# Kernel tuning notes

Measured on AMD Instinct MI355X. Metric: run time of the kernel, lower is better.

The kernel has to match this reference:

```python
import jax, jax.numpy as jnp
import numpy as np

DIM_HEAD = 64
NB_FEATURES = 256
COND_LEN = 128
NUM_CHUNKS = 128  # torch .chunk(128, dim=-2) -> 128 chunks
KERNEL_EPS = 1e-4
ATTN_EPS = 1e-6


def gaussian_orthogonal_random_matrix(key, nb_rows, nb_cols):
    # scaling == 0 branch of the torch code
    nb_full = nb_rows // nb_cols
    blocks = []
    for i in range(nb_full + (1 if nb_rows % nb_cols else 0)):
        g = jax.random.normal(jax.random.fold_in(key, i), (nb_cols, nb_cols), dtype=jnp.float32)
        qm, _ = jnp.linalg.qr(g)
        blocks.append(qm.T)
    final = jnp.concatenate(blocks, axis=0)[:nb_rows]
    mult = jnp.linalg.norm(
        jax.random.normal(jax.random.fold_in(key, 10_000), (nb_rows, nb_cols), dtype=jnp.float32), axis=1)
    return mult[:, None] * final  # diag(mult) @ final


def softmax_kernel(x, proj, is_query):
    d = x.shape[-1]
    data_normalizer = d ** (-0.25)
    ratio = proj.shape[0] ** (-0.5)
    # [b,h,n,m]
    data_dash = jnp.einsum('bhnd,md->bhnm', data_normalizer * x, proj)
    diag = (x * x).sum(-1) * 0.5 * (data_normalizer ** 2)  # [b,h,n]
    diag = diag[..., None]
    if is_query:
        m = jnp.max(data_dash, axis=-1, keepdims=True)
    else:
        m = jnp.max(data_dash)
    return ratio * (jnp.exp(data_dash - diag - m) + KERNEL_EPS)


def causal_linear_attention(qf, kf, v):
    b, h, s, m = qf.shape
    e = v.shape[-1]
    # conditioning prefix: non-causal linear attention
    cq, ck, cv = qf[:, :, :COND_LEN], kf[:, :, :COND_LEN], v[:, :, :COND_LEN]
    cond_k_sum = ck.sum(axis=-2)                                   # [b,h,m]
    cond_Dinv = 1.0 / jnp.einsum('bhnd,bhd->bhn', cq, cond_k_sum)
    cond_ctx = jnp.einsum('bhnd,bhne->bhde', ck, cv)               # [b,h,m,e]
    cond_out = jnp.einsum('bhde,bhnd,bhn->bhne', cond_ctx, cq, cond_Dinv)

    # causal chunked recurrence over the remainder
    rest = s - COND_LEN
    L = rest // NUM_CHUNKS
    def to_chunks(t):
        return t[:, :, COND_LEN:].reshape(b, h, NUM_CHUNKS, L, t.shape[-1]).transpose(2, 0, 1, 3, 4)
    qr, kr, vr = to_chunks(qf), to_chunks(kf), to_chunks(v)

    def step(carry, qkv):
        last_k, last_ctx = carry  # [b,h,m], [b,h,m,e]
        qc, kc, vc = qkv          # [b,h,L,m], [b,h,L,m], [b,h,L,e]
        k_cumsum = last_k[:, :, None, :] + jnp.cumsum(kc, axis=-2)
        D_inv = 1.0 / jnp.einsum('bhld,bhld->bhl', qc, k_cumsum + ATTN_EPS)
        ctx = jnp.einsum('bhld,bhle->bhlde', kc, vc)
        ctx_cumsum = last_ctx[:, :, None] + jnp.cumsum(ctx, axis=-3)
        out = jnp.einsum('bhlde,bhld,bhl->bhle', ctx_cumsum, qc, D_inv)
        return (k_cumsum[:, :, -1], ctx_cumsum[:, :, -1]), out

    _, outs = jax.lax.scan(step, (cond_k_sum, cond_ctx), (qr, kr, vr))
    outs = outs.transpose(1, 2, 0, 3, 4).reshape(b, h, rest, e)
    return jnp.concatenate([cond_out, outs], axis=2)


def setup_inputs() -> dict:
    key = jax.random.key(0)
    kq, kk, kv, kp = jax.random.split(key, 4)
    B, H, S = 4, 16, 4096
    q = jax.random.normal(kq, (B, H, S, DIM_HEAD), dtype=jnp.float32)
    k = jax.random.normal(kk, (B, H, S, DIM_HEAD), dtype=jnp.float32)
    v = jax.random.normal(kv, (B, H, S, DIM_HEAD), dtype=jnp.float32)
    projection_matrix = gaussian_orthogonal_random_matrix(kp, NB_FEATURES, DIM_HEAD)
    return {"q": q, "k": k, "v": v, "projection_matrix": projection_matrix}


def reference(q, k, v, projection_matrix):
    qf = softmax_kernel(q, projection_matrix, is_query=True)
    kf = softmax_kernel(k, projection_matrix, is_query=False)
    return causal_linear_attention(qf, kf, v)
```

## Files before the change

### kernel.cpp

```cpp
#include <hip/hip_runtime.h>
#include <math.h>


#define S_TOT 4096
#define CONDL 128
#define SLOT_F 16640
#define RATIO 0.0625f
#define DNORM 0.35355339059327378f
#define KEPS  1e-4f
#define AEPS  1e-6f

typedef __attribute__((ext_vector_type(8))) short bf16x8;
typedef __attribute__((ext_vector_type(2))) unsigned uint2v;
typedef __attribute__((ext_vector_type(4))) float f32x4;

#define MFMA16(a,b,c) __builtin_amdgcn_mfma_f32_16x16x32_bf16(a,b,c,0,0,0)

static __device__ __forceinline__ unsigned cvtpk(float a, float b){
    unsigned r;
    asm("v_cvt_pk_bf16_f32 %0, %1, %2" : "=v"(r) : "v"(a), "v"(b));
    return r;
}
static __device__ __forceinline__ float lo16f(unsigned u){ return __uint_as_float(u << 16); }
static __device__ __forceinline__ float hi16f(unsigned u){ return __uint_as_float(u & 0xffff0000u); }

static __device__ __forceinline__ unsigned short f2bh(float x){
    unsigned u = __float_as_uint(x);
    u += 0x7fffu + ((u >> 16) & 1u);
    return (unsigned short)(u >> 16);
}
static __device__ __forceinline__ float bh2f(unsigned short h){
    return __uint_as_float((unsigned)h << 16);
}
static __device__ __forceinline__ unsigned packhl(float x){
    unsigned u1 = cvtpk(x, x);
    float r = x - lo16f(u1);
    return cvtpk(x, r);
}
static __device__ __forceinline__ void unpk(const uint4 a, const uint4 b, bf16x8& h, bf16x8& l){
    h[0]=(short)a.x; h[1]=(short)a.y; h[2]=(short)a.z; h[3]=(short)a.w;
    h[4]=(short)b.x; h[5]=(short)b.y; h[6]=(short)b.z; h[7]=(short)b.w;
    l[0]=(short)(a.x>>16); l[1]=(short)(a.y>>16); l[2]=(short)(a.z>>16); l[3]=(short)(a.w>>16);
    l[4]=(short)(b.x>>16); l[5]=(short)(b.y>>16); l[6]=(short)(b.z>>16); l[7]=(short)(b.w>>16);
}
static __device__ __forceinline__ unsigned mapf(float x){
    unsigned u = __float_as_uint(x);
    return (u & 0x80000000u) ? ~u : (u | 0x80000000u);
}
static __device__ __forceinline__ float unmapf(unsigned u){
    return __uint_as_float((u & 0x80000000u) ? (u ^ 0x80000000u) : ~u);
}

static __device__ __forceinline__ void conv_write(const float* __restrict__ Xg, long r0,
        int tid, short (*Xh)[64][8], short (*Xl)[64][8], float* __restrict__ diag_)
{
    int row = tid >> 4;
    int c4  = (tid & 15) * 4;
    float4 x4 = *(const float4*)(Xg + (r0 + row)*64 + c4);
    float x0 = x4.x*DNORM, x1 = x4.y*DNORM, x2 = x4.z*DNORM, x3 = x4.w*DNORM;
    float ss = x0*x0 + x1*x1 + x2*x2 + x3*x3;
    ss += __shfl_xor(ss, 1, 64);
    ss += __shfl_xor(ss, 2, 64);
    ss += __shfl_xor(ss, 4, 64);
    ss += __shfl_xor(ss, 8, 64);
    if ((tid & 15) == 0) diag_[row] = 0.5f * ss;
    int rt = row >> 4, lr = row & 15;
    int kk = c4 >> 5, c5 = c4 & 31;
    int fg, j0;
    if (c5 < 16){ fg = c5 >> 2; j0 = 0; } else { fg = (c5 - 16) >> 2; j0 = 4; }
    int f = kk*2 + rt;
    unsigned a01 = cvtpk(x0, x1), a23 = cvtpk(x2, x3);
    unsigned b01 = cvtpk(x0 - lo16f(a01), x1 - hi16f(a01));
    unsigned b23 = cvtpk(x2 - lo16f(a23), x3 - hi16f(a23));
    uint2v hv, lv;
    hv[0] = a01; hv[1] = a23;
    lv[0] = b01; lv[1] = b23;
    *(uint2v*)&Xh[f][fg*16 + lr][j0] = hv;
    *(uint2v*)&Xl[f][fg*16 + lr][j0] = lv;
}

static __device__ __forceinline__ void load_pfrags(const unsigned short* __restrict__ Ph,
        const unsigned short* __restrict__ Pl, int w, int l15, int g,
        bf16x8 (&Pfh)[2][2], bf16x8 (&Pfl)[2][2])
{
#pragma unroll
    for (int mt=0; mt<2; mt++)
#pragma unroll
      for (int kk=0; kk<2; kk++){
        const unsigned short* ph = Ph + (w*32 + mt*16 + l15)*64 + kk*32 + g*4;
        const unsigned short* pl = Pl + (w*32 + mt*16 + l15)*64 + kk*32 + g*4;
        bf16x8 fh, fl;
#pragma unroll
        for (int j=0;j<4;j++){
            fh[j]=(short)ph[j]; fh[4+j]=(short)ph[16+j];
            fl[j]=(short)pl[j]; fl[4+j]=(short)pl[16+j];
        }
        Pfh[mt][kk]=fh; Pfl[mt][kk]=fl;
      }
}

static __device__ __forceinline__ void dd_frags(const short (*Xh)[64][8], const short (*Xl)[64][8],
        int lane, const bf16x8 (&Pfh)[2][2], const bf16x8 (&Pfl)[2][2], f32x4 (&acc)[2][2])
{
#pragma unroll
    for (int rt=0;rt<2;rt++)
#pragma unroll
      for (int mt=0;mt<2;mt++) acc[rt][mt] = f32x4{0.f,0.f,0.f,0.f};
#pragma unroll
    for (int kk=0;kk<2;kk++)
#pragma unroll
      for (int rt=0;rt<2;rt++){
        bf16x8 xh = *(const bf16x8*)&Xh[kk*2+rt][lane][0];
        bf16x8 xl = *(const bf16x8*)&Xl[kk*2+rt][lane][0];
#pragma unroll
        for (int mt=0;mt<2;mt++){
            acc[rt][mt] = MFMA16(xh, Pfh[mt][kk], acc[rt][mt]);
            acc[rt][mt] = MFMA16(xh, Pfl[mt][kk], acc[rt][mt]);
            acc[rt][mt] = MFMA16(xl, Pfh[mt][kk], acc[rt][mt]);
        }
      }
}

static __device__ __forceinline__ void dd_frags_g(const short (*Xh)[64][8], const short (*Xl)[64][8],
        int lane, int w, const unsigned short* __restrict__ Pfh, const unsigned short* __restrict__ Pfl,
        f32x4 (&acc)[2][2])
{
#pragma unroll
    for (int rr=0;rr<2;rr++)
#pragma unroll
      for (int mt=0;mt<2;mt++) acc[rr][mt] = f32x4{0.f,0.f,0.f,0.f};
#pragma unroll
    for (int kk=0;kk<2;kk++){
        bf16x8 ph[2], pl[2];
#pragma unroll
        for (int mt=0;mt<2;mt++){
            int f = w*4 + kk*2 + mt;
            ph[mt] = *(const bf16x8*)(Pfh + (f*64 + lane)*8);
            pl[mt] = *(const bf16x8*)(Pfl + (f*64 + lane)*8);
        }
#pragma unroll
        for (int rr=0;rr<2;rr++){
            bf16x8 xh = *(const bf16x8*)&Xh[kk*2+rr][lane][0];
            bf16x8 xl = *(const bf16x8*)&Xl[kk*2+rr][lane][0];
#pragma unroll
            for (int mt=0;mt<2;mt++){
                acc[rr][mt] = MFMA16(xh, ph[mt], acc[rr][mt]);
                acc[rr][mt] = MFMA16(xh, pl[mt], acc[rr][mt]);
                acc[rr][mt] = MFMA16(xl, ph[mt], acc[rr][mt]);
            }
        }
    }
}

static __device__ __forceinline__ void sfrag(const f32x4 a, const f32x4 b, bf16x8& h, bf16x8& l){
    union U { bf16x8 v; unsigned u[4]; } H, L;
    H.u[0] = cvtpk(a[0], a[1]); H.u[1] = cvtpk(a[2], a[3]);
    H.u[2] = cvtpk(b[0], b[1]); H.u[3] = cvtpk(b[2], b[3]);
    L.u[0] = cvtpk(a[0] - lo16f(H.u[0]), a[1] - hi16f(H.u[0]));
    L.u[1] = cvtpk(a[2] - lo16f(H.u[1]), a[3] - hi16f(H.u[1]));
    L.u[2] = cvtpk(b[0] - lo16f(H.u[2]), b[1] - hi16f(H.u[2]));
    L.u[3] = cvtpk(b[2] - lo16f(H.u[3]), b[3] - hi16f(H.u[3]));
    h = H.v; l = L.v;
}

static __device__ __forceinline__ void inter_half(const unsigned* __restrict__ qf_,
        const f32x4 (&S)[8], int rt, int l15, int g, int xsw,
        f32x4 &Cp0, f32x4 &Cp1)
{
#pragma unroll
    for (int ktl=0; ktl<4; ktl++){
        int ft = rt*4 + ktl;
        bf16x8 sh, sl; sfrag(S[2*ktl], S[2*ktl+1], sh, sl);
        {
            int rowb = l15*256;
            uint4 q0 = *(const uint4*)&qf_[rowb + ((ft*32 + g*4) ^ xsw)];
            uint4 q1 = *(const uint4*)&qf_[rowb + ((ft*32 + 16 + g*4) ^ xsw)];
            bf16x8 qh, ql; unpk(q0, q1, qh, ql);
            Cp0 = MFMA16(qh, sh, Cp0);
            Cp0 = MFMA16(qh, sl, Cp0);
            Cp0 = MFMA16(ql, sh, Cp0);
        }
        {
            int rowb = (16 + l15)*256;
            uint4 q0 = *(const uint4*)&qf_[rowb + ((ft*32 + g*4) ^ xsw)];
            uint4 q1 = *(const uint4*)&qf_[rowb + ((ft*32 + 16 + g*4) ^ xsw)];
            bf16x8 qh, ql; unpk(q0, q1, qh, ql);
            Cp1 = MFMA16(qh, sh, Cp1);
            Cp1 = MFMA16(qh, sl, Cp1);
            Cp1 = MFMA16(ql, sh, Cp1);
        }
    }
}

__global__ __launch_bounds__(256) void init_p_kernel(const float* __restrict__ proj,
        unsigned short* __restrict__ Ph, unsigned short* __restrict__ Pl,
        unsigned short* __restrict__ Pfh, unsigned short* __restrict__ Pfl){
    int i = blockIdx.x*256 + threadIdx.x;
    float x = proj[i];
    unsigned short h = f2bh(x);
    unsigned short l = f2bh(x - bh2f(h));
    Ph[i] = h;
    Pl[i] = l;
    int m = i >> 6, d = i & 63;
    int w = m >> 5, mt = (m >> 4) & 1, l15 = m & 15;
    int kk = d >> 5, r5 = d & 31;
    int half = r5 >> 4, g = (r5 & 15) >> 2, jj = r5 & 3;
    int f = w*4 + kk*2 + mt, lane = g*16 + l15, j = half*4 + jj;
    int o = (f*64 + lane)*8 + j;
    Pfh[o] = h; Pfl[o] = l;
}

__global__ __launch_bounds__(256) void kmax_kernel(const float* __restrict__ k,
        const unsigned short* __restrict__ Ph, unsigned* __restrict__ kmax_u){
    __shared__ float red[4];
    int tid = threadIdx.x;
    int lane = tid & 63, w = tid >> 6;
    int l15 = lane & 15, g = lane >> 4;
    long r0 = (long)blockIdx.x * 32;
    bf16x8 xh[2][2];
#pragma unroll
    for (int kk=0;kk<2;kk++)
#pragma unroll
      for (int rt=0;rt<2;rt++){
        const float* rp = k + (r0 + rt*16 + l15)*64 + kk*32 + g*4;
        float4 a = *(const float4*)rp;
        float4 b = *(const float4*)(rp + 16);
        float xs[8] = {a.x,a.y,a.z,a.w,b.x,b.y,b.z,b.w};
#pragma unroll
        for (int j=0;j<8;j++) xh[kk][rt][j] = (short)f2bh(xs[j]*DNORM);
      }
    float mx = -1e30f;
#pragma unroll
    for (int mtl=0; mtl<4; mtl++){
        int mtile = w*4 + mtl;
        bf16x8 pf[2];
#pragma unroll
        for (int kk=0;kk<2;kk++){
            const unsigned short* ph = Ph + (mtile*16 + l15)*64 + kk*32 + g*4;
#pragma unroll
            for (int j=0;j<4;j++){ pf[kk][j]=(short)ph[j]; pf[kk][4+j]=(short)ph[16+j]; }
        }
        f32x4 acc[2] = {f32x4{0.f,0.f,0.f,0.f}, f32x4{0.f,0.f,0.f,0.f}};
#pragma unroll
        for (int kk=0;kk<2;kk++)
#pragma unroll
          for (int rt=0;rt<2;rt++)
            acc[rt] = MFMA16(xh[kk][rt], pf[kk], acc[rt]);
#pragma unroll
        for (int rt=0;rt<2;rt++)
#pragma unroll
          for (int i=0;i<4;i++) mx = fmaxf(mx, acc[rt][i]);
    }
#pragma unroll
    for (int d=1; d<64; d<<=1) mx = fmaxf(mx, __shfl_xor(mx, d, 64));
    if (lane == 0) red[w] = mx;
    __syncthreads();
    if (tid == 0){
        float m2 = fmaxf(fmaxf(red[0],red[1]), fmaxf(red[2],red[3]));
        atomicMax(kmax_u, mapf(m2));
    }
}

__global__ __launch_bounds__(512, 2) void b_kernel(const float* __restrict__ k,
        const float* __restrict__ v,
        const unsigned short* __restrict__ Ph, const unsigned short* __restrict__ Pl,
        const unsigned* __restrict__ kmax_u, float* __restrict__ states,
        int CH, int nch){
    __shared__ short Xh[4][64][8], Xl[4][64][8];
    __shared__ unsigned kf_mt[256][36];
    __shared__ unsigned Vt_u[64][36];
    __shared__ float diagk_[32];
    int tid = threadIdx.x;
    int lane = tid & 63, w = tid >> 6;
    int l15 = lane & 15, g = lane >> 4;
    int cx = blockIdx.x, bh = blockIdx.y;
    int o = (cx == 0) ? 0 : CONDL + (cx-1)*CH;
    int nsub = ((cx == 0) ? CONDL : CH) >> 5;
    long rowbase = (long)bh * S_TOT + o;
    float kmax = unmapf(*kmax_u);
    bf16x8 Pfh[2][2], Pfl[2][2];
    load_pfrags(Ph, Pl, w, l15, g, Pfh, Pfl);
    f32x4 Sacc[2][4];
#pragma unroll
    for (int mt=0;mt<2;mt++)
#pragma unroll
      for (int et=0;et<4;et++) Sacc[mt][et] = f32x4{0.f,0.f,0.f,0.f};
    float zacc[2] = {0.f, 0.f};

    for (int st = 0; st < nsub; st++){
        long r0 = rowbase + st*32;
        conv_write(k, r0, tid, Xh, Xl, diagk_);
        {
            int t = tid >> 4, e4 = (tid & 15)*4;
            float4 v4 = *(const float4*)(v + (r0 + t)*64 + e4);
            Vt_u[e4+0][t] = packhl(v4.x);
            Vt_u[e4+1][t] = packhl(v4.y);
            Vt_u[e4+2][t] = packhl(v4.z);
            Vt_u[e4+3][t] = packhl(v4.w);
        }
        __syncthreads();
        f32x4 dk[2][2];
        dd_frags(Xh, Xl, lane, Pfh, Pfl, dk);
        float zd[2] = {0.f, 0.f};
#pragma unroll
        for (int rt=0;rt<2;rt++)
#pragma unroll
          for (int i=0;i<4;i++){
            int t = rt*16 + g*4 + i;
            float dg = diagk_[t];
#pragma unroll
            for (int mt=0;mt<2;mt++){
                float kv = RATIO * (__expf(dk[rt][mt][i] - dg - kmax) + KEPS);
                kf_mt[w*32 + mt*16 + l15][t] = packhl(kv);
                zd[mt] += kv;
            }
          }
#pragma unroll
        for (int mt=0;mt<2;mt++){
            zd[mt] += __shfl_xor(zd[mt], 16, 64);
            zd[mt] += __shfl_xor(zd[mt], 32, 64);
            zacc[mt] += zd[mt];
        }
        __syncthreads();
#pragma unroll
        for (int mt=0;mt<2;mt++){
            int m = (w*2 + mt)*16 + l15;
            const uint4* kp0 = (const uint4*)&kf_mt[m][g*4];
            const uint4* kp1 = (const uint4*)&kf_mt[m][16 + g*4];
            bf16x8 kh, kl; unpk(*kp0, *kp1, kh, kl);
#pragma unroll
            for (int et=0;et<4;et++){
                const uint4* vp0 = (const uint4*)&Vt_u[et*16 + l15][g*4];
                const uint4* vp1 = (const uint4*)&Vt_u[et*16 + l15][16 + g*4];
                bf16x8 vh, vl; unpk(*vp0, *vp1, vh, vl);
                Sacc[mt][et] = MFMA16(kh, vh, Sacc[mt][et]);
                Sacc[mt][et] = MFMA16(kh, vl, Sacc[mt][et]);
                Sacc[mt][et] = MFMA16(kl, vh, Sacc[mt][et]);
            }
        }
        __syncthreads();
    }
    float* Sg = states + ((long)(bh*nch + cx)) * SLOT_F;
#pragma unroll
    for (int mt=0;mt<2;mt++)
#pragma unroll
      for (int et=0;et<4;et++)
#pragma unroll
        for (int i=0;i<4;i++)
            Sg[((w*2+mt)*16 + g*4 + i)*64 + et*16 + l15] = Sacc[mt][et][i];
    if (g == 0){
        Sg[16384 + w*32 + l15]      = zacc[0];
        Sg[16384 + w*32 + 16 + l15] = zacc[1];
    }
}

__global__ __launch_bounds__(256) void scan_kernel(float* __restrict__ states, int nch){
    int idx = blockIdx.x*256 + threadIdx.x;
    if (idx >= SLOT_F) return;
    float* base = states + (long)blockIdx.y * nch * SLOT_F + idx;
    float prev = 0.f;
    for (int c = 0; c < nch; c++){
        float t = base[(long)c * SLOT_F];
        base[(long)c * SLOT_F] = prev;
        prev += t;
    }
}

__global__ __launch_bounds__(512, 2) void d_kernel(const float* __restrict__ q,
        const float* __restrict__ k, const float* __restrict__ v,
        const unsigned short* __restrict__ Pfh, const unsigned short* __restrict__ Pfl,
        const unsigned* __restrict__ kmax_u, const float* __restrict__ states,
        float* __restrict__ out, int CH, int nch){
    __shared__ __attribute__((aligned(16))) unsigned lds_[18496];
    unsigned* qf_ = lds_;
    unsigned* kf_ = lds_ + 8192;
    unsigned* XA_ = lds_ + 16384;
    float*   den_ = (float*)(lds_ + 18432);
    float*   dgk_ = (float*)(lds_ + 18464);
    float*   dgq_ = (float*)kf_;
    unsigned* rmax_ = kf_ + 32;
    unsigned* A_ = XA_;
    float*   xch_ = (float*)(lds_ + 17408);
    short (*Xh)[64][8] = (short (*)[64][8])XA_;
    short (*Xl)[64][8] = (short (*)[64][8])(XA_ + 1024);

    int tid = threadIdx.x;
    int lane = tid & 63, w = tid >> 6;
    int l15 = lane & 15, g = lane >> 4;
    int et = w & 3, rt = w >> 2;
    bool owner = (rt == 0);
    int cx = blockIdx.x, bh = blockIdx.y;
    bool causal = (cx > 0);
    int o = causal ? (CONDL + (cx-1)*CH) : 0;
    int nsub = (causal ? CH : CONDL) >> 5;
    float epsv = causal ? AEPS : 0.f;
    int slot = causal ? cx : 1;
    const float* Sg = states + ((long)(bh*nch + slot)) * SLOT_F;
    long rowbase = (long)bh * S_TOT + o;
    float kmax = unmapf(*kmax_u);
    int xsw = (l15 & 7) << 2;

    f32x4 S[8];
#pragma unroll
    for (int Mtl=0; Mtl<8; Mtl++){
#pragma unroll
        for (int i=0;i<4;i++)
            S[Mtl][i] = Sg[((rt*8 + Mtl)*16 + g*4 + i)*64 + et*16 + l15];
    }
    float z0 = Sg[16384 + w*32 + l15];
    float z1 = Sg[16384 + w*32 + 16 + l15];

    for (int st = 0; st < nsub; st++){
        long r0 = rowbase + st*32;
        conv_write(q, r0, tid, Xh, Xl, dgq_);
        if (tid < 32){ den_[tid] = 0.f; rmax_[tid] = 0u; }
        __syncthreads();
        f32x4 dq[2][2];
        dd_frags_g(Xh, Xl, lane, w, Pfh, Pfl, dq);
#pragma unroll
        for (int rr=0;rr<2;rr++)
#pragma unroll
          for (int i=0;i<4;i++){
            float mx = fmaxf(dq[rr][0][i], dq[rr][1][i]);
            mx = fmaxf(mx, __shfl_xor(mx, 1, 64));
            mx = fmaxf(mx, __shfl_xor(mx, 2, 64));
            mx = fmaxf(mx, __shfl_xor(mx, 4, 64));
            mx = fmaxf(mx, __shfl_xor(mx, 8, 64));
            if (l15 == 0) atomicMax(&rmax_[rr*16 + g*4 + i], mapf(mx));
          }
        __syncthreads();
        {
#pragma unroll
            for (int rr=0;rr<2;rr++)
#pragma unroll
              for (int i=0;i<4;i++){
                int row = rr*16 + g*4 + i;
                float dgv = dgq_[row];
                float rm = unmapf(rmax_[row]);
                float s1p = 0.f, s2p = 0.f;
#pragma unroll
                for (int mt=0;mt<2;mt++){
                    float qv = RATIO * (__expf(dq[rr][mt][i] - dgv - rm) + KEPS);
                    s1p += qv;
                    s2p += qv * (mt ? z1 : z0);
                    int m = w*32 + mt*16 + l15;
                    qf_[row*256 + (m ^ ((row & 7) << 2))] = packhl(qv);
                }
#pragma unroll
                for (int d2=1; d2<16; d2<<=1){
                    s1p += __shfl_xor(s1p, d2, 64);
                    s2p += __shfl_xor(s2p, d2, 64);
                }
                if (l15 == 0) atomicAdd(&den_[row], s2p + epsv * s1p);
              }
        }
        if (causal) conv_write(k, r0, tid, Xh, Xl, dgk_);
        __syncthreads();
        if (causal){
            f32x4 dk[2][2];
            dd_frags_g(Xh, Xl, lane, w, Pfh, Pfl, dk);
            float zd0 = 0.f, zd1 = 0.f;
#pragma unroll
            for (int rr=0;rr<2;rr++){
                float dg0 = dgk_[rr*16 + g*4 + 0];
                float dg1 = dgk_[rr*16 + g*4 + 1];
                float dg2 = dgk_[rr*16 + g*4 + 2];
                float dg3 = dgk_[rr*16 + g*4 + 3];
#pragma unroll
                for (int mt=0;mt<2;mt++){
                    float k0 = RATIO * (__expf(dk[rr][mt][0] - dg0 - kmax) + KEPS);
                    float k1 = RATIO * (__expf(dk[rr][mt][1] - dg1 - kmax) + KEPS);
                    float k2 = RATIO * (__expf(dk[rr][mt][2] - dg2 - kmax) + KEPS);
                    float k3 = RATIO * (__expf(dk[rr][mt][3] - dg3 - kmax) + KEPS);
                    if (mt == 0) zd0 += k0+k1+k2+k3; else zd1 += k0+k1+k2+k3;
                    uint4 kw;
                    kw.x = packhl(k0); kw.y = packhl(k1);
                    kw.z = packhl(k2); kw.w = packhl(k3);
                    int m = w*32 + mt*16 + l15;
                    *(uint4*)&kf_[m*32 + ((rr*16 + g*4) ^ xsw)] = kw;
                }
            }
            zd0 += __shfl_xor(zd0, 16, 64); zd0 += __shfl_xor(zd0, 32, 64);
            zd1 += __shfl_xor(zd1, 16, 64); zd1 += __shfl_xor(zd1, 32, 64);
            z0 += zd0; z1 += zd1;
        }
        __syncthreads();
        float vv[8];
        if (causal){
            const float* vb = v + r0*64 + et*16 + l15;
#pragma unroll
            for (int p2=0;p2<2;p2++)
#pragma unroll
              for (int j=0;j<4;j++)
                vv[p2*4+j] = vb[(p2*16 + g*4 + j)*64];
        }
        f32x4 Cp0{0.f,0.f,0.f,0.f}, Cp1{0.f,0.f,0.f,0.f};
        if (owner){
            if (causal){
                int ar = et >> 1, tt = et & 1;
                f32x4 c{0.f,0.f,0.f,0.f};
                int rowb = (ar*16 + l15)*256;
#pragma unroll
                for (int kt=0;kt<8;kt++){
                    uint4 q0 = *(const uint4*)&qf_[rowb + ((kt*32 + g*4) ^ xsw)];
                    uint4 q1 = *(const uint4*)&qf_[rowb + ((kt*32 + 16 + g*4) ^ xsw)];
                    bf16x8 qh, ql; unpk(q0, q1, qh, ql);
                    bf16x8 kh, kl;
#pragma unroll
                    for (int p2=0;p2<2;p2++)
#pragma unroll
                      for (int j=0;j<4;j++){
                        int m = kt*32 + p2*16 + g*4 + j;
                        unsigned u = kf_[m*32 + ((tt*16 + l15) ^ ((m & 7) << 2))];
                        kh[p2*4+j] = (short)u;
                        kl[p2*4+j] = (short)(u >> 16);
                      }
                    c = MFMA16(qh, kh, c);
                    c = MFMA16(qh, kl, c);
                    c = MFMA16(ql, kh, c);
                }
                int t = tt*16 + l15;
#pragma unroll
                for (int i=0;i<4;i++){
                    int r = ar*16 + g*4 + i;
                    float a = (t <= r) ? c[i] : 0.f;
                    A_[r*32 + (t ^ ((r & 7) << 2))] = packhl(a);
                    float p = a;
                    p += __shfl_xor(p, 1, 64);
                    p += __shfl_xor(p, 2, 64);
                    p += __shfl_xor(p, 4, 64);
                    p += __shfl_xor(p, 8, 64);
                    if (l15 == 0) atomicAdd(&den_[r], p);
                }
            }
        } else {
            inter_half(qf_, S, rt, l15, g, xsw, Cp0, Cp1);
            *(float4*)&xch_[(et*64 + lane)*4] = float4{Cp0[0],Cp0[1],Cp0[2],Cp0[3]};
        }
        __syncthreads();
        if (owner){
            inter_half(qf_, S, rt, l15, g, xsw, Cp0, Cp1);
            float4 pp = *(const float4*)&xch_[(et*64 + lane)*4];
            Cp0[0] += pp.x; Cp0[1] += pp.y; Cp0[2] += pp.z; Cp0[3] += pp.w;
            *(float4*)&xch_[(et*64 + lane)*4] = float4{Cp1[0],Cp1[1],Cp1[2],Cp1[3]};
        }
        if (causal){
            f32x4 va{vv[0], vv[1], vv[2], vv[3]};
            f32x4 vb2{vv[4], vv[5], vv[6], vv[7]};
            bf16x8 vh, vl; sfrag(va, vb2, vh, vl);
#pragma unroll
            for (int Mtl=0;Mtl<8;Mtl++){
                int mb = ((rt*8 + Mtl)*16 + l15)*32;
                uint4 k0 = *(const uint4*)&kf_[mb + ((g*4) ^ xsw)];
                uint4 k1 = *(const uint4*)&kf_[mb + ((16 + g*4) ^ xsw)];
                bf16x8 kh, kl; unpk(k0, k1, kh, kl);
                S[Mtl] = MFMA16(kh, vh, S[Mtl]);
                S[Mtl] = MFMA16(kh, vl, S[Mtl]);
                S[Mtl] = MFMA16(kl, vh, S[Mtl]);
            }
            int rb = (rt*16 + l15)*32;
            uint4 a0 = *(const uint4*)&A_[rb + ((g*4) ^ xsw)];
            uint4 a1 = *(const uint4*)&A_[rb + ((16 + g*4) ^ xsw)];
            bf16x8 ah, al; unpk(a0, a1, ah, al);
            f32x4& Ct = owner ? Cp0 : Cp1;
            Ct = MFMA16(ah, vh, Ct);
            Ct = MFMA16(ah, vl, Ct);
            Ct = MFMA16(al, vh, Ct);
        }
        if (owner){
#pragma unroll
            for (int i=0;i<4;i++){
                int row = g*4 + i;
                out[(r0 + row)*64 + et*16 + l15] = Cp0[i] / den_[row];
            }
        }
        __syncthreads();
        if (!owner){
            float4 pp = *(const float4*)&xch_[(et*64 + lane)*4];
            Cp1[0] += pp.x; Cp1[1] += pp.y; Cp1[2] += pp.z; Cp1[3] += pp.w;
#pragma unroll
            for (int i=0;i<4;i++){
                int row = 16 + g*4 + i;
                out[(r0 + row)*64 + et*16 + l15] = Cp1[i] / den_[row];
            }
        }
        __syncthreads();
    }
}

extern "C" void kernel_launch(void* const* d_in, const int* in_sizes, int n_in,
                              void* d_out, int out_size, void* d_ws, size_t ws_size,
                              hipStream_t stream) {
    const float* q = (const float*)d_in[0];
    const float* k = (const float*)d_in[1];
    const float* v = (const float*)d_in[2];
    const float* proj = (const float*)d_in[3];
    float* out = (float*)d_out;

    unsigned* kmax_u = (unsigned*)d_ws;
    unsigned short* Ph  = (unsigned short*)((char*)d_ws + 256);
    unsigned short* Pl  = Ph + 16384;
    unsigned short* Pfh = Pl + 16384;
    unsigned short* Pfl = Pfh + 16384;
    float* states = (float*)((char*)d_ws + 256 + 131072);
    size_t fixed = 256 + 131072;

    int CH, nch;
    size_t need128 = fixed + (size_t)64 * 32 * SLOT_F * 4;
    if (ws_size >= need128){ CH = 128; nch = 32; }
    else                  { CH = 992; nch = 5;  }

    hipMemsetAsync(d_ws, 0, 4, stream);
    hipLaunchKernelGGL(init_p_kernel, dim3(64), dim3(256), 0, stream, proj, Ph, Pl, Pfh, Pfl);
    hipLaunchKernelGGL(kmax_kernel, dim3(8192), dim3(256), 0, stream, k, Ph, kmax_u);
    hipLaunchKernelGGL(b_kernel, dim3(nch, 64), dim3(512), 0, stream, k, v, Ph, Pl, kmax_u, states, CH, nch);
    hipLaunchKernelGGL(scan_kernel, dim3(65, 64), dim3(256), 0, stream, states, nch);
    hipLaunchKernelGGL(d_kernel, dim3(nch, 64), dim3(512), 0, stream, q, k, v, Pfh, Pfl, kmax_u, states, out, CH, nch);
}
```

Measured before the change: 639.6 us.

## Split bf16 hi/lo planes in LDS and add transposed K feature copy

Stores q/k features and the intra-chunk A matrix in LDS as separate high and low bf16 planes, with k-major index permutations. MFMA operands can then be loaded as contiguous 16-byte vectors instead of being unpacked from interleaved hi/lo words. A transposed copy of the k features is also written so the QK^T product reads contiguous rows rather than gathering 16 scalar LDS reads per fragment. The LDS footprint grows to about 107 KB and launch bounds drop to one block per CU, so occupancy falls in exchange for fewer LDS instructions and less unpack work.

```diff
diff --git a/kernel.cpp b/kernel.cpp
--- a/kernel.cpp
+++ b/kernel.cpp
@@ -163,28 +163,26 @@
     h = H.v; l = L.v;
 }
 
-static __device__ __forceinline__ void inter_half(const unsigned* __restrict__ qf_,
-        const f32x4 (&S)[8], int rt, int l15, int g, int xsw,
+static __device__ __forceinline__ void inter_half(const unsigned short* __restrict__ qfh_,
+        const unsigned short* __restrict__ qfl_,
+        const f32x4 (&S)[8], int rt, int l15, int g, int xq,
         f32x4 &Cp0, f32x4 &Cp1)
 {
 #pragma unroll
     for (int ktl=0; ktl<4; ktl++){
         int ft = rt*4 + ktl;
         bf16x8 sh, sl; sfrag(S[2*ktl], S[2*ktl+1], sh, sl);
+        int fo = (ft*32 + g*8) ^ xq;
         {
-            int rowb = l15*256;
-            uint4 q0 = *(const uint4*)&qf_[rowb + ((ft*32 + g*4) ^ xsw)];
-            uint4 q1 = *(const uint4*)&qf_[rowb + ((ft*32 + 16 + g*4) ^ xsw)];
-            bf16x8 qh, ql; unpk(q0, q1, qh, ql);
+            bf16x8 qh = *(const bf16x8*)&qfh_[l15*256 + fo];
+            bf16x8 ql = *(const bf16x8*)&qfl_[l15*256 + fo];
             Cp0 = MFMA16(qh, sh, Cp0);
             Cp0 = MFMA16(qh, sl, Cp0);
             Cp0 = MFMA16(ql, sh, Cp0);
         }
         {
-            int rowb = (16 + l15)*256;
-            uint4 q0 = *(const uint4*)&qf_[rowb + ((ft*32 + g*4) ^ xsw)];
-            uint4 q1 = *(const uint4*)&qf_[rowb + ((ft*32 + 16 + g*4) ^ xsw)];
-            bf16x8 qh, ql; unpk(q0, q1, qh, ql);
+            bf16x8 qh = *(const bf16x8*)&qfh_[(16 + l15)*256 + fo];
+            bf16x8 ql = *(const bf16x8*)&qfl_[(16 + l15)*256 + fo];
             Cp1 = MFMA16(qh, sh, Cp1);
             Cp1 = MFMA16(qh, sl, Cp1);
             Cp1 = MFMA16(ql, sh, Cp1);
@@ -366,23 +364,27 @@
     }
 }
 
-__global__ __launch_bounds__(512, 2) void d_kernel(const float* __restrict__ q,
+__global__ __launch_bounds__(512, 1) void d_kernel(const float* __restrict__ q,
         const float* __restrict__ k, const float* __restrict__ v,
         const unsigned short* __restrict__ Pfh, const unsigned short* __restrict__ Pfl,
         const unsigned* __restrict__ kmax_u, const float* __restrict__ states,
         float* __restrict__ out, int CH, int nch){
-    __shared__ __attribute__((aligned(16))) unsigned lds_[18496];
-    unsigned* qf_ = lds_;
-    unsigned* kf_ = lds_ + 8192;
-    unsigned* XA_ = lds_ + 16384;
-    float*   den_ = (float*)(lds_ + 18432);
-    float*   dgk_ = (float*)(lds_ + 18464);
-    float*   dgq_ = (float*)kf_;
-    unsigned* rmax_ = kf_ + 32;
-    unsigned* A_ = XA_;
-    float*   xch_ = (float*)(lds_ + 17408);
-    short (*Xh)[64][8] = (short (*)[64][8])XA_;
-    short (*Xl)[64][8] = (short (*)[64][8])(XA_ + 1024);
+    __shared__ __attribute__((aligned(16))) unsigned short hws[53504];
+    unsigned short* qfh_ = hws;
+    unsigned short* qfl_ = hws + 8192;
+    unsigned short* kfh_ = hws + 16384;
+    unsigned short* kfl_ = hws + 24576;
+    unsigned short* kfTh_ = hws + 32768;
+    unsigned short* kfTl_ = hws + 40960;
+    short (*Xh)[64][8] = (short (*)[64][8])(hws + 49152);
+    short (*Xl)[64][8] = (short (*)[64][8])(hws + 51200);
+    unsigned short* Ah_ = hws + 49152;
+    unsigned short* Al_ = hws + 50176;
+    float* xch_ = (float*)(hws + 51200);
+    float* den_ = (float*)(hws + 53248);
+    float* dgq_ = (float*)(hws + 53312);
+    float* dgk_ = (float*)(hws + 53376);
+    unsigned* rmax_ = (unsigned*)(hws + 53440);
 
     int tid = threadIdx.x;
     int lane = tid & 63, w = tid >> 6;
@@ -398,7 +400,9 @@
     const float* Sg = states + ((long)(bh*nch + slot)) * SLOT_F;
     long rowbase = (long)bh * S_TOT + o;
     float kmax = unmapf(*kmax_u);
-    int xsw = (l15 & 7) << 2;
+    int xq = (l15 & 7) << 3;
+    int xk = (l15 & 3) << 3;
+    int pbase = w*32 + ((l15 >> 2) << 3) + (l15 & 3);
 
     f32x4 S[8];
 #pragma unroll
@@ -437,14 +441,19 @@
                 int row = rr*16 + g*4 + i;
                 float dgv = dgq_[row];
                 float rm = unmapf(rmax_[row]);
+                int xrow = ((g*4 + i) & 7) << 3;
                 float s1p = 0.f, s2p = 0.f;
 #pragma unroll
                 for (int mt=0;mt<2;mt++){
                     float qv = RATIO * (__expf(dq[rr][mt][i] - dgv - rm) + KEPS);
                     s1p += qv;
                     s2p += qv * (mt ? z1 : z0);
-                    int m = w*32 + mt*16 + l15;
-                    qf_[row*256 + (m ^ ((row & 7) << 2))] = packhl(qv);
+                    unsigned hu = cvtpk(qv, qv);
+                    float lres = qv - lo16f(hu);
+                    unsigned lu = cvtpk(lres, lres);
+                    int idx = row*256 + ((pbase + mt*4) ^ xrow);
+                    qfh_[idx] = (unsigned short)hu;
+                    qfl_[idx] = (unsigned short)lu;
                 }
 #pragma unroll
                 for (int d2=1; d2<16; d2<<=1){
@@ -473,11 +482,26 @@
                     float k2 = RATIO * (__expf(dk[rr][mt][2] - dg2 - kmax) + KEPS);
                     float k3 = RATIO * (__expf(dk[rr][mt][3] - dg3 - kmax) + KEPS);
                     if (mt == 0) zd0 += k0+k1+k2+k3; else zd1 += k0+k1+k2+k3;
-                    uint4 kw;
-                    kw.x = packhl(k0); kw.y = packhl(k1);
-                    kw.z = packhl(k2); kw.w = packhl(k3);
+                    unsigned h01 = cvtpk(k0, k1), h23 = cvtpk(k2, k3);
+                    float l0 = k0 - lo16f(h01), l1 = k1 - hi16f(h01);
+                    float l2 = k2 - lo16f(h23), l3 = k3 - hi16f(h23);
+                    unsigned L01 = cvtpk(l0, l1), L23 = cvtpk(l2, l3);
                     int m = w*32 + mt*16 + l15;
-                    *(uint4*)&kf_[m*32 + ((rr*16 + g*4) ^ xsw)] = kw;
+                    int bidx = m*32 + ((g*8 + rr*4) ^ xk);
+                    uint2v hv; hv[0] = h01; hv[1] = h23;
+                    *(uint2v*)&kfh_[bidx] = hv;
+                    uint2v lv2; lv2[0] = L01; lv2[1] = L23;
+                    *(uint2v*)&kfl_[bidx] = lv2;
+                    int pm = pbase + mt*4;
+                    int t0 = rr*16 + g*4;
+                    kfTh_[(t0+0)*256 + (pm ^ ((((g*4)+0)&7)<<3))] = (unsigned short)h01;
+                    kfTh_[(t0+1)*256 + (pm ^ ((((g*4)+1)&7)<<3))] = (unsigned short)(h01>>16);
+                    kfTh_[(t0+2)*256 + (pm ^ ((((g*4)+2)&7)<<3))] = (unsigned short)h23;
+                    kfTh_[(t0+3)*256 + (pm ^ ((((g*4)+3)&7)<<3))] = (unsigned short)(h23>>16);
+                    kfTl_[(t0+0)*256 + (pm ^ ((((g*4)+0)&7)<<3))] = (unsigned short)L01;
+                    kfTl_[(t0+1)*256 + (pm ^ ((((g*4)+1)&7)<<3))] = (unsigned short)(L01>>16);
+                    kfTl_[(t0+2)*256 + (pm ^ ((((g*4)+2)&7)<<3))] = (unsigned short)L23;
+                    kfTl_[(t0+3)*256 + (pm ^ ((((g*4)+3)&7)<<3))] = (unsigned short)(L23>>16);
                 }
             }
             zd0 += __shfl_xor(zd0, 16, 64); zd0 += __shfl_xor(zd0, 32, 64);
@@ -498,33 +522,31 @@
         if (owner){
             if (causal){
                 int ar = et >> 1, tt = et & 1;
+                int t = tt*16 + l15;
+                int rowA = ar*16 + l15;
                 f32x4 c{0.f,0.f,0.f,0.f};
-                int rowb = (ar*16 + l15)*256;
 #pragma unroll
                 for (int kt=0;kt<8;kt++){
-                    uint4 q0 = *(const uint4*)&qf_[rowb + ((kt*32 + g*4) ^ xsw)];
-                    uint4 q1 = *(const uint4*)&qf_[rowb + ((kt*32 + 16 + g*4) ^ xsw)];
-                    bf16x8 qh, ql; unpk(q0, q1, qh, ql);
-                    bf16x8 kh, kl;
-#pragma unroll
-                    for (int p2=0;p2<2;p2++)
-#pragma unroll
-                      for (int j=0;j<4;j++){
-                        int m = kt*32 + p2*16 + g*4 + j;
-                        unsigned u = kf_[m*32 + ((tt*16 + l15) ^ ((m & 7) << 2))];
-                        kh[p2*4+j] = (short)u;
-                        kl[p2*4+j] = (short)(u >> 16);
-                      }
+                    int fo = (kt*32 + g*8) ^ xq;
+                    bf16x8 qh = *(const bf16x8*)&qfh_[rowA*256 + fo];
+                    bf16x8 ql = *(const bf16x8*)&qfl_[rowA*256 + fo];
+                    bf16x8 kh = *(const bf16x8*)&kfTh_[t*256 + fo];
+                    bf16x8 kl = *(const bf16x8*)&kfTl_[t*256 + fo];
                     c = MFMA16(qh, kh, c);
                     c = MFMA16(qh, kl, c);
                     c = MFMA16(ql, kh, c);
                 }
-                int t = tt*16 + l15;
+                int pt5 = tt*4 + ((l15 & 12) << 1) + (l15 & 3);
 #pragma unroll
                 for (int i=0;i<4;i++){
                     int r = ar*16 + g*4 + i;
                     float a = (t <= r) ? c[i] : 0.f;
-                    A_[r*32 + (t ^ ((r & 7) << 2))] = packhl(a);
+                    unsigned hu = cvtpk(a, a);
+                    float lres = a - lo16f(hu);
+                    unsigned lu = cvtpk(lres, lres);
+                    int idx = r*32 + (pt5 ^ ((((g*4)+i)&3)<<3));
+                    Ah_[idx] = (unsigned short)hu;
+                    Al_[idx] = (unsigned short)lu;
                     float p = a;
                     p += __shfl_xor(p, 1, 64);
                     p += __shfl_xor(p, 2, 64);
@@ -534,12 +556,12 @@
                 }
             }
         } else {
-            inter_half(qf_, S, rt, l15, g, xsw, Cp0, Cp1);
+            inter_half(qfh_, qfl_, S, rt, l15, g, xq, Cp0, Cp1);
             *(float4*)&xch_[(et*64 + lane)*4] = float4{Cp0[0],Cp0[1],Cp0[2],Cp0[3]};
         }
         __syncthreads();
         if (owner){
-            inter_half(qf_, S, rt, l15, g, xsw, Cp0, Cp1);
+            inter_half(qfh_, qfl_, S, rt, l15, g, xq, Cp0, Cp1);
             float4 pp = *(const float4*)&xch_[(et*64 + lane)*4];
             Cp0[0] += pp.x; Cp0[1] += pp.y; Cp0[2] += pp.z; Cp0[3] += pp.w;
             *(float4*)&xch_[(et*64 + lane)*4] = float4{Cp1[0],Cp1[1],Cp1[2],Cp1[3]};
@@ -550,18 +572,18 @@
             bf16x8 vh, vl; sfrag(va, vb2, vh, vl);
 #pragma unroll
             for (int Mtl=0;Mtl<8;Mtl++){
-                int mb = ((rt*8 + Mtl)*16 + l15)*32;
-                uint4 k0 = *(const uint4*)&kf_[mb + ((g*4) ^ xsw)];
-                uint4 k1 = *(const uint4*)&kf_[mb + ((16 + g*4) ^ xsw)];
-                bf16x8 kh, kl; unpk(k0, k1, kh, kl);
+                int m = (rt*8 + Mtl)*16 + l15;
+                int bi = m*32 + ((g*8) ^ xk);
+                bf16x8 kh = *(const bf16x8*)&kfh_[bi];
+                bf16x8 kl = *(const bf16x8*)&kfl_[bi];
                 S[Mtl] = MFMA16(kh, vh, S[Mtl]);
                 S[Mtl] = MFMA16(kh, vl, S[Mtl]);
                 S[Mtl] = MFMA16(kl, vh, S[Mtl]);
             }
-            int rb = (rt*16 + l15)*32;
-            uint4 a0 = *(const uint4*)&A_[rb + ((g*4) ^ xsw)];
-            uint4 a1 = *(const uint4*)&A_[rb + ((16 + g*4) ^ xsw)];
-            bf16x8 ah, al; unpk(a0, a1, ah, al);
+            int r = rt*16 + l15;
+            int ai = r*32 + ((g*8) ^ xk);
+            bf16x8 ah = *(const bf16x8*)&Ah_[ai];
+            bf16x8 al = *(const bf16x8*)&Al_[ai];
             f32x4& Ct = owner ? Cp0 : Cp1;
             Ct = MFMA16(ah, vh, Ct);
             Ct = MFMA16(ah, vl, Ct);
```

After: 663.2 us. +3.7%, slower.

## Keep projection fragments in registers, prefetch q/k, add transposed k-feature LDS copy

Applied to the files above, without the earlier changes.

Projection fragments are loaded into registers once per block instead of being re-read from global memory for every sub-tile. The next q tile and the current k tile are prefetched into registers so the loads overlap with compute. A transposed copy of the k features is written to a new LDS buffer, letting the intra-chunk QK^T MFMA read k with two vector loads instead of eight scalar gathers. In exchange LDS use grows to about 104KB and launch bounds drop to one block per CU, which lowers occupancy.

```diff
diff --git a/kernel.cpp b/kernel.cpp
--- a/kernel.cpp
+++ b/kernel.cpp
@@ -51,12 +51,11 @@
     return __uint_as_float((u & 0x80000000u) ? (u ^ 0x80000000u) : ~u);
 }
 
-static __device__ __forceinline__ void conv_write(const float* __restrict__ Xg, long r0,
-        int tid, short (*Xh)[64][8], short (*Xl)[64][8], float* __restrict__ diag_)
+static __device__ __forceinline__ void conv_store(float4 x4, int tid,
+        short (*Xh)[64][8], short (*Xl)[64][8], float* __restrict__ diag_)
 {
     int row = tid >> 4;
     int c4  = (tid & 15) * 4;
-    float4 x4 = *(const float4*)(Xg + (r0 + row)*64 + c4);
     float x0 = x4.x*DNORM, x1 = x4.y*DNORM, x2 = x4.z*DNORM, x3 = x4.w*DNORM;
     float ss = x0*x0 + x1*x1 + x2*x2 + x3*x3;
     ss += __shfl_xor(ss, 1, 64);
@@ -79,6 +78,15 @@
     *(uint2v*)&Xl[f][fg*16 + lr][j0] = lv;
 }
 
+static __device__ __forceinline__ void conv_write(const float* __restrict__ Xg, long r0,
+        int tid, short (*Xh)[64][8], short (*Xl)[64][8], float* __restrict__ diag_)
+{
+    int row = tid >> 4;
+    int c4  = (tid & 15) * 4;
+    float4 x4 = *(const float4*)(Xg + (r0 + row)*64 + c4);
+    conv_store(x4, tid, Xh, Xl, diag_);
+}
+
 static __device__ __forceinline__ void load_pfrags(const unsigned short* __restrict__ Ph,
         const unsigned short* __restrict__ Pl, int w, int l15, int g,
         bf16x8 (&Pfh)[2][2], bf16x8 (&Pfl)[2][2])
@@ -99,6 +107,20 @@
       }
 }
 
+static __device__ __forceinline__ void load_pfrags_fm(const unsigned short* __restrict__ Pfh,
+        const unsigned short* __restrict__ Pfl, int w, int lane,
+        bf16x8 (&Ph_r)[2][2], bf16x8 (&Pl_r)[2][2])
+{
+#pragma unroll
+    for (int kk=0; kk<2; kk++)
+#pragma unroll
+      for (int mt=0; mt<2; mt++){
+        int f = w*4 + kk*2 + mt;
+        Ph_r[mt][kk] = *(const bf16x8*)(Pfh + (f*64 + lane)*8);
+        Pl_r[mt][kk] = *(const bf16x8*)(Pfl + (f*64 + lane)*8);
+      }
+}
+
 static __device__ __forceinline__ void dd_frags(const short (*Xh)[64][8], const short (*Xl)[64][8],
         int lane, const bf16x8 (&Pfh)[2][2], const bf16x8 (&Pfl)[2][2], f32x4 (&acc)[2][2])
 {
@@ -119,37 +141,6 @@
             acc[rt][mt] = MFMA16(xl, Pfh[mt][kk], acc[rt][mt]);
         }
       }
-}
-
-static __device__ __forceinline__ void dd_frags_g(const short (*Xh)[64][8], const short (*Xl)[64][8],
-        int lane, int w, const unsigned short* __restrict__ Pfh, const unsigned short* __restrict__ Pfl,
-        f32x4 (&acc)[2][2])
-{
-#pragma unroll
-    for (int rr=0;rr<2;rr++)
-#pragma unroll
-      for (int mt=0;mt<2;mt++) acc[rr][mt] = f32x4{0.f,0.f,0.f,0.f};
-#pragma unroll
-    for (int kk=0;kk<2;kk++){
-        bf16x8 ph[2], pl[2];
-#pragma unroll
-        for (int mt=0;mt<2;mt++){
-            int f = w*4 + kk*2 + mt;
-            ph[mt] = *(const bf16x8*)(Pfh + (f*64 + lane)*8);
-            pl[mt] = *(const bf16x8*)(Pfl + (f*64 + lane)*8);
-        }
-#pragma unroll
-        for (int rr=0;rr<2;rr++){
-            bf16x8 xh = *(const bf16x8*)&Xh[kk*2+rr][lane][0];
-            bf16x8 xl = *(const bf16x8*)&Xl[kk*2+rr][lane][0];
-#pragma unroll
-            for (int mt=0;mt<2;mt++){
-                acc[rr][mt] = MFMA16(xh, ph[mt], acc[rr][mt]);
-                acc[rr][mt] = MFMA16(xh, pl[mt], acc[rr][mt]);
-                acc[rr][mt] = MFMA16(xl, ph[mt], acc[rr][mt]);
-            }
-        }
-    }
 }
 
 static __device__ __forceinline__ void sfrag(const f32x4 a, const f32x4 b, bf16x8& h, bf16x8& l){
@@ -366,21 +357,22 @@
     }
 }
 
-__global__ __launch_bounds__(512, 2) void d_kernel(const float* __restrict__ q,
+__global__ __launch_bounds__(512, 1) void d_kernel(const float* __restrict__ q,
         const float* __restrict__ k, const float* __restrict__ v,
         const unsigned short* __restrict__ Pfh, const unsigned short* __restrict__ Pfl,
         const unsigned* __restrict__ kmax_u, const float* __restrict__ states,
         float* __restrict__ out, int CH, int nch){
-    __shared__ __attribute__((aligned(16))) unsigned lds_[18496];
-    unsigned* qf_ = lds_;
-    unsigned* kf_ = lds_ + 8192;
-    unsigned* XA_ = lds_ + 16384;
-    float*   den_ = (float*)(lds_ + 18432);
-    float*   dgk_ = (float*)(lds_ + 18464);
+    __shared__ __attribute__((aligned(16))) unsigned lds_[26688];
+    unsigned* qf_  = lds_;
+    unsigned* kf_  = lds_ + 8192;
+    unsigned* kfT_ = lds_ + 16384;
+    unsigned* XA_  = lds_ + 24576;
+    float*   den_ = (float*)(lds_ + 26624);
+    float*   dgk_ = (float*)(lds_ + 26656);
     float*   dgq_ = (float*)kf_;
     unsigned* rmax_ = kf_ + 32;
     unsigned* A_ = XA_;
-    float*   xch_ = (float*)(lds_ + 17408);
+    float*   xch_ = (float*)(XA_ + 1024);
     short (*Xh)[64][8] = (short (*)[64][8])XA_;
     short (*Xl)[64][8] = (short (*)[64][8])(XA_ + 1024);
 
@@ -400,6 +392,9 @@
     float kmax = unmapf(*kmax_u);
     int xsw = (l15 & 7) << 2;
 
+    bf16x8 Ph_r[2][2], Pl_r[2][2];
+    load_pfrags_fm(Pfh, Pfl, w, lane, Ph_r, Pl_r);
+
     f32x4 S[8];
 #pragma unroll
     for (int Mtl=0; Mtl<8; Mtl++){
@@ -410,13 +405,19 @@
     float z0 = Sg[16384 + w*32 + l15];
     float z1 = Sg[16384 + w*32 + 16 + l15];
 
+    const float* qptr = q + rowbase*64 + (tid >> 4)*64 + (tid & 15)*4;
+    const float* kptr = k + rowbase*64 + (tid >> 4)*64 + (tid & 15)*4;
+    float4 qpre = *(const float4*)qptr;
+
     for (int st = 0; st < nsub; st++){
         long r0 = rowbase + st*32;
-        conv_write(q, r0, tid, Xh, Xl, dgq_);
+        float4 kpre;
+        if (causal) kpre = *(const float4*)(kptr + st*2048);
+        conv_store(qpre, tid, Xh, Xl, dgq_);
         if (tid < 32){ den_[tid] = 0.f; rmax_[tid] = 0u; }
         __syncthreads();
         f32x4 dq[2][2];
-        dd_frags_g(Xh, Xl, lane, w, Pfh, Pfl, dq);
+        dd_frags(Xh, Xl, lane, Ph_r, Pl_r, dq);
 #pragma unroll
         for (int rr=0;rr<2;rr++)
 #pragma unroll
@@ -454,11 +455,11 @@
                 if (l15 == 0) atomicAdd(&den_[row], s2p + epsv * s1p);
               }
         }
-        if (causal) conv_write(k, r0, tid, Xh, Xl, dgk_);
+        if (causal) conv_store(kpre, tid, Xh, Xl, dgk_);
         __syncthreads();
         if (causal){
             f32x4 dk[2][2];
-            dd_frags_g(Xh, Xl, lane, w, Pfh, Pfl, dk);
+            dd_frags(Xh, Xl, lane, Ph_r, Pl_r, dk);
             float zd0 = 0.f, zd1 = 0.f;
 #pragma unroll
             for (int rr=0;rr<2;rr++){
@@ -478,6 +479,12 @@
                     kw.z = packhl(k2); kw.w = packhl(k3);
                     int m = w*32 + mt*16 + l15;
                     *(uint4*)&kf_[m*32 + ((rr*16 + g*4) ^ xsw)] = kw;
+                    int t0r = rr*16 + g*4;
+                    int mm = m;
+                    kfT_[(t0r+0)*256 + (mm ^ ((((g*4)+0) & 7) << 2))] = kw.x;
+                    kfT_[(t0r+1)*256 + (mm ^ ((((g*4)+1) & 7) << 2))] = kw.y;
+                    kfT_[(t0r+2)*256 + (mm ^ ((((g*4)+2) & 7) << 2))] = kw.z;
+                    kfT_[(t0r+3)*256 + (mm ^ ((((g*4)+3) & 7) << 2))] = kw.w;
                 }
             }
             zd0 += __shfl_xor(zd0, 16, 64); zd0 += __shfl_xor(zd0, 32, 64);
@@ -485,6 +492,7 @@
             z0 += zd0; z1 += zd1;
         }
         __syncthreads();
+        if (st + 1 < nsub) qpre = *(const float4*)(qptr + (st+1)*2048);
         float vv[8];
         if (causal){
             const float* vb = v + r0*64 + et*16 + l15;
@@ -498,6 +506,8 @@
         if (owner){
             if (causal){
                 int ar = et >> 1, tt = et & 1;
+                int t = tt*16 + l15;
+                int tb = t*256;
                 f32x4 c{0.f,0.f,0.f,0.f};
                 int rowb = (ar*16 + l15)*256;
 #pragma unroll
@@ -505,21 +515,13 @@
                     uint4 q0 = *(const uint4*)&qf_[rowb + ((kt*32 + g*4) ^ xsw)];
                     uint4 q1 = *(const uint4*)&qf_[rowb + ((kt*32 + 16 + g*4) ^ xsw)];
                     bf16x8 qh, ql; unpk(q0, q1, qh, ql);
-                    bf16x8 kh, kl;
-#pragma unroll
-                    for (int p2=0;p2<2;p2++)
-#pragma unroll
-                      for (int j=0;j<4;j++){
-                        int m = kt*32 + p2*16 + g*4 + j;
-                        unsigned u = kf_[m*32 + ((tt*16 + l15) ^ ((m & 7) << 2))];
-                        kh[p2*4+j] = (short)u;
-                        kl[p2*4+j] = (short)(u >> 16);
-                      }
+                    uint4 kt0 = *(const uint4*)&kfT_[tb + ((kt*32 + g*4) ^ xsw)];
+                    uint4 kt1 = *(const uint4*)&kfT_[tb + ((kt*32 + 16 + g*4) ^ xsw)];
+                    bf16x8 kh, kl; unpk(kt0, kt1, kh, kl);
                     c = MFMA16(qh, kh, c);
                     c = MFMA16(qh, kl, c);
                     c = MFMA16(ql, kh, c);
                 }
-                int t = tt*16 + l15;
 #pragma unroll
                 for (int i=0;i<4;i++){
                     int r = ar*16 + g*4 + i;
```

After: 640.2 us. About the same (+0.1%).
